# Kernel optimization log

Hardware: AMD Instinct MI355X
Metric: run time of the kernel (lower is better)

Reference implementation:

```python
import jax, jax.numpy as jnp
import numpy as np

E, H, K = 768, 512, 8  # word_emb_size, nhidden, nhead
B, NA, NC = 32, 64, 64


def setup_inputs() -> dict:
    key = jax.random.key(0)
    ks = jax.random.split(key, 8)
    w = lambda k, shape: (jax.random.normal(k, shape, jnp.float32) * 0.02)
    return {
        'he_anchor': jax.random.normal(ks[0], (B, NA, E), jnp.float32),
        'he_pos': jax.random.normal(ks[1], (B, NC, E), jnp.float32),
        'he_neg': jax.random.uniform(ks[2], (B,), jnp.float32),  # SBERT target scores
        'Wa': w(ks[3], (H, E)), 'ba': jnp.zeros((H,), jnp.float32),
        'Wc': w(ks[4], (H, E)), 'bc': jnp.zeros((H,), jnp.float32),
        'Watt': w(ks[5], (K, H)), 'batt': jnp.zeros((K,), jnp.float32),
        'Wscore': w(ks[6], (1, K * H)), 'bscore': jnp.zeros((1,), jnp.float32),
    }


def _score(ha, hc, Wa, ba, Wc, bc, Watt, batt, Wscore, bscore):
    b, na, _ = ha.shape
    A = ha @ Wa.T + ba  # [B,Na,H]  (a2h)
    C = hc @ Wc.T + bc  # [B,Nc,H]  (c2h)
    # self_mul[b,i,j,h] = A[b,i,h]*C[b,j,h]; att logits = h2att(self_mul)
    logits = jnp.einsum('bih,bjh,kh->bkij', A, C, Watt) + batt[None, :, None, None]
    att = jax.nn.softmax(logits.reshape(b, K, -1), axis=-1).reshape(logits.shape)  # [B,K,Na,Nc]
    # per-head bilinear: out[b,k,h] = sum_ij A[b,i,h] * att[b,k,i,j] * C[b,j,h]
    out = jnp.einsum('bih,bkij,bjh->bkh', A, att, C)  # [B,K,H], head-major like torch cat
    score = out.reshape(b, K * H) @ Wscore.T + bscore  # [B,1]
    return score, att


def reference(he_anchor, he_pos, he_neg, Wa, ba, Wc, bc, Watt, batt, Wscore, bscore):
    score_p, att_map = _score(he_anchor, he_pos, Wa, ba, Wc, bc, Watt, batt, Wscore, bscore)
    score_bert = he_neg.reshape(-1, 1)
    loss = jnp.mean((score_p - score_bert) ** 2)  # nn.MSELoss
    return score_p, loss, att_map
```

## Files before the change

### kernel.cpp

```cpp
#include <hip/hip_runtime.h>

#define E_DIM 768

typedef __attribute__((ext_vector_type(8))) short bf16x8;
typedef __attribute__((ext_vector_type(4))) float f32x4;

__device__ __forceinline__ unsigned short f2bf(float f) {
    union { float f; unsigned int u; } v; v.f = f;
    unsigned int u = v.u;
    return (unsigned short)((u + 0x7FFFu + ((u >> 16) & 1u)) >> 16);
}
__device__ __forceinline__ float bfu_lo(unsigned int u) {
    union { unsigned int u; float f; } v; v.u = u << 16; return v.f;
}
__device__ __forceinline__ float bfu_hi(unsigned int u) {
    union { unsigned int u; float f; } v; v.u = u & 0xFFFF0000u; return v.f;
}
__device__ __forceinline__ float bfs(unsigned short s) {
    union { unsigned int u; float f; } v; v.u = ((unsigned int)s) << 16; return v.f;
}
__device__ __forceinline__ unsigned int cvt_pk_bf16(float lo, float hi) {
    unsigned int u;
    asm("v_cvt_pk_bf16_f32 %0, %1, %2" : "=v"(u) : "v"(lo), "v"(hi));
    return u;
}

__global__ __launch_bounds__(512) void k_proj_mfma(
    const float* __restrict__ he_a, const float* __restrict__ Wa, const float* __restrict__ ba,
    const float* __restrict__ he_p, const float* __restrict__ Wc, const float* __restrict__ bc,
    unsigned short* __restrict__ dsts, float* __restrict__ score_acc,
    unsigned int* __restrict__ counter)
{
    __shared__ unsigned short Xs[128 * 40];
    __shared__ unsigned short Wl[64 * 40];
    int t = threadIdx.x;
    int bid = blockIdx.x;
    if (bid == 0) {
        if (t < 32) score_acc[t] = 0.f;
        else if (t == 32) *counter = 0u;
    }
    int which = bid >> 7;
    int loc = bid & 127;
    int mbase = (loc & 15) * 128;
    int hbase = (loc >> 4) * 64;
    const float* Xg = which ? he_p : he_a;
    const float* Wg = which ? Wc : Wa;
    const float* bias = which ? bc : ba;
    int lane = t & 63, w = t >> 6;
    int wr = w >> 1, wc = w & 1;

    int xr0 = t >> 3,          xc0 = t & 7;
    int xr1 = (t + 512) >> 3,  xc1 = t & 7;
    int wrr = t >> 3,          wcc = t & 7;

    float4 p0 = *(const float4*)(Xg + (size_t)(mbase + xr0) * E_DIM + xc0 * 4);
    float4 p1 = *(const float4*)(Xg + (size_t)(mbase + xr1) * E_DIM + xc1 * 4);
    float4 p2 = *(const float4*)(Wg + (size_t)(hbase + wrr) * E_DIM + wcc * 4);

    f32x4 acc[2][2] = {};
    for (int kt = 0; kt < 24; ++kt) {
        __syncthreads();
        *(uint2*)&Xs[xr0 * 40 + xc0 * 4] =
            make_uint2(cvt_pk_bf16(p0.x, p0.y), cvt_pk_bf16(p0.z, p0.w));
        *(uint2*)&Xs[xr1 * 40 + xc1 * 4] =
            make_uint2(cvt_pk_bf16(p1.x, p1.y), cvt_pk_bf16(p1.z, p1.w));
        *(uint2*)&Wl[wrr * 40 + wcc * 4] =
            make_uint2(cvt_pk_bf16(p2.x, p2.y), cvt_pk_bf16(p2.z, p2.w));
        if (kt < 23) {
            int e0 = (kt + 1) * 32;
            p0 = *(const float4*)(Xg + (size_t)(mbase + xr0) * E_DIM + e0 + xc0 * 4);
            p1 = *(const float4*)(Xg + (size_t)(mbase + xr1) * E_DIM + e0 + xc1 * 4);
            p2 = *(const float4*)(Wg + (size_t)(hbase + wrr) * E_DIM + e0 + wcc * 4);
        }
        __syncthreads();
        int ar = lane & 15;
        int k0 = (lane >> 4) * 8;
        bf16x8 af[2], bfr[2];
#pragma unroll
        for (int mi = 0; mi < 2; ++mi)
            af[mi] = *(const bf16x8*)&Xs[(wr * 32 + mi * 16 + ar) * 40 + k0];
#pragma unroll
        for (int ni = 0; ni < 2; ++ni)
            bfr[ni] = *(const bf16x8*)&Wl[(wc * 32 + ni * 16 + ar) * 40 + k0];
#pragma unroll
        for (int mi = 0; mi < 2; ++mi)
#pragma unroll
            for (int ni = 0; ni < 2; ++ni)
                acc[mi][ni] = __builtin_amdgcn_mfma_f32_16x16x32_bf16(
                    af[mi], bfr[ni], acc[mi][ni], 0, 0, 0);
    }
#pragma unroll
    for (int ni = 0; ni < 2; ++ni) {
        int h = hbase + wc * 32 + ni * 16 + (lane & 15);
        float bv = bias[h];
#pragma unroll
        for (int mi = 0; mi < 2; ++mi) {
#pragma unroll
            for (int r = 0; r < 4; ++r) {
                int grow = mbase + wr * 32 + mi * 16 + (lane >> 4) * 4 + r;
                int b = grow >> 6, i = grow & 63;
                float v = acc[mi][ni][r] + bv;
                dsts[(size_t)b * 65536 + (which ? 32768 : 0) + i * 512 + h] = f2bf(v);
            }
        }
    }
}

__global__ __launch_bounds__(512) void k_att_fused(
    float* __restrict__ out, const unsigned short* __restrict__ src,
    const float* __restrict__ Watt, const float* __restrict__ Wsc,
    const float* __restrict__ he_neg, const float* __restrict__ bsc,
    float* __restrict__ score_acc, unsigned int* __restrict__ counter)
{
    __shared__ float red[8];
    __shared__ float sqv[32];
    __shared__ int lastflag;
    int t = threadIdx.x;
    int lane = t & 63, w = t >> 6;
    int rf = w & 3, jh = w >> 2;
    int b = blockIdx.x & 31, k = blockIdx.x >> 5;
    int l15 = lane & 15, lhi = lane >> 4;

    const unsigned short* Ab = src + (size_t)b * 65536;
    const unsigned short* Cb = Ab + 32768;
    const unsigned short* ap  = Ab + (size_t)(rf * 16 + l15) * 512 + lhi * 8;
    const unsigned short* cp0 = Cb + (size_t)(jh * 32 + l15) * 512 + lhi * 8;
    const unsigned short* cp1 = cp0 + 16 * 512;
    const float* wkbase = Watt + k * 512 + lhi * 8;
    const float* wgbase = Wsc  + k * 512 + lhi * 8;

    f32x4 accS[2] = {}, accG[2] = {};
#pragma unroll 2
    for (int ks = 0; ks < 16; ++ks) {
        int h = ks * 32;
        bf16x8 af  = *(const bf16x8*)(ap + h);
        bf16x8 cb0 = *(const bf16x8*)(cp0 + h);
        bf16x8 cb1 = *(const bf16x8*)(cp1 + h);
        float wkv[8], wgv[8];
        *(float4*)&wkv[0] = *(const float4*)(wkbase + h);
        *(float4*)&wkv[4] = *(const float4*)(wkbase + h + 4);
        *(float4*)&wgv[0] = *(const float4*)(wgbase + h);
        *(float4*)&wgv[4] = *(const float4*)(wgbase + h + 4);
        float a[8];
#pragma unroll
        for (int e = 0; e < 8; ++e) a[e] = bfs((unsigned short)af[e]);
        union { unsigned int u[4]; bf16x8 v; } ak, ag;
#pragma unroll
        for (int e2 = 0; e2 < 4; ++e2) {
            ak.u[e2] = cvt_pk_bf16(a[2 * e2] * wkv[2 * e2], a[2 * e2 + 1] * wkv[2 * e2 + 1]);
            ag.u[e2] = cvt_pk_bf16(a[2 * e2] * wgv[2 * e2], a[2 * e2 + 1] * wgv[2 * e2 + 1]);
        }
        accS[0] = __builtin_amdgcn_mfma_f32_16x16x32_bf16(ak.v, cb0, accS[0], 0, 0, 0);
        accS[1] = __builtin_amdgcn_mfma_f32_16x16x32_bf16(ak.v, cb1, accS[1], 0, 0, 0);
        accG[0] = __builtin_amdgcn_mfma_f32_16x16x32_bf16(ag.v, cb0, accG[0], 0, 0, 0);
        accG[1] = __builtin_amdgcn_mfma_f32_16x16x32_bf16(ag.v, cb1, accG[1], 0, 0, 0);
    }

    float lmax = accS[0][0];
#pragma unroll
    for (int ni = 0; ni < 2; ++ni)
#pragma unroll
        for (int r = 0; r < 4; ++r) lmax = fmaxf(lmax, accS[ni][r]);
    float v = lmax;
#pragma unroll
    for (int off = 32; off > 0; off >>= 1) v = fmaxf(v, __shfl_xor(v, off));
    if (lane == 0) red[w] = v;
    __syncthreads();
    float M = red[0];
#pragma unroll
    for (int q = 1; q < 8; ++q) M = fmaxf(M, red[q]);
    __syncthreads();
    float ev[8];
    float lsum = 0.f;
#pragma unroll
    for (int ni = 0; ni < 2; ++ni)
#pragma unroll
        for (int r = 0; r < 4; ++r) {
            float e = __expf(accS[ni][r] - M);
            ev[ni * 4 + r] = e;
            lsum += e;
        }
    v = lsum;
#pragma unroll
    for (int off = 32; off > 0; off >>= 1) v += __shfl_xor(v, off);
    if (lane == 0) red[w] = v;
    __syncthreads();
    float Z = 0.f;
#pragma unroll
    for (int q = 0; q < 8; ++q) Z += red[q];
    float inv = 1.0f / Z;
    __syncthreads();

    float pacc = 0.f;
    float* attk = out + 33 + (size_t)b * 32768 + (size_t)k * 4096;
#pragma unroll
    for (int ni = 0; ni < 2; ++ni) {
        int j = jh * 32 + ni * 16 + l15;
#pragma unroll
        for (int r = 0; r < 4; ++r) {
            int i = rf * 16 + lhi * 4 + r;
            float av = ev[ni * 4 + r] * inv;
            attk[i * 64 + j] = av;
            pacc += av * accG[ni][r];
        }
    }
    v = pacc;
#pragma unroll
    for (int off = 32; off > 0; off >>= 1) v += __shfl_xor(v, off);
    if (lane == 0) red[w] = v;
    __syncthreads();
    if (t == 0) {
        float tot = 0.f;
#pragma unroll
        for (int q = 0; q < 8; ++q) tot += red[q];
        atomicAdd(&score_acc[b], tot);
        __threadfence();
        unsigned int done = atomicAdd(counter, 1u);
        lastflag = (done == 255u) ? 1 : 0;
    }
    __syncthreads();
    if (lastflag) {
        __threadfence();
        if (t < 32) {
            float s = atomicAdd(&score_acc[t], 0.0f) + bsc[0];
            out[t] = s;
            float d = s - he_neg[t];
            sqv[t] = d * d;
        }
        __syncthreads();
        if (t == 0) {
            float l = 0.f;
            for (int q = 0; q < 32; ++q) l += sqv[q];
            out[32] = l * (1.0f / 32.0f);
        }
    }
}

__global__ __launch_bounds__(256) void k_att_valu8(
    float* __restrict__ out, const unsigned int* __restrict__ src,
    const float* __restrict__ Watt, const float* __restrict__ Wsc)
{
    __shared__ unsigned int Al[64 * 260];
    __shared__ unsigned int Cl[64 * 260];
    __shared__ float Wattl[512], Wscl[512];
    __shared__ float red[4];
    int t = threadIdx.x;
    int lane = t & 63, wave = t >> 6;
    int b = blockIdx.x;
    const unsigned int* srcb = src + (size_t)b * 32768;

    for (int s = t; s < 16384; s += 256) {
        int row = s >> 8, hp = s & 255;
        Al[row * 260 + hp] = srcb[s];
        Cl[row * 260 + hp] = srcb[16384 + s];
    }

    int i = t >> 2;
    int jb = (t & 3) * 16;
    float* attreg = out + 33 + (size_t)b * 32768;
    float blocktotal = 0.f;

    for (int k = 0; k < 8; ++k) {
        for (int s = t; s < 512; s += 256) {
            Wattl[s] = Watt[k * 512 + s];
            Wscl[s]  = Wsc[k * 512 + s];
        }
        __syncthreads();
        float sacc[16] = {}, gacc[16] = {};
        const unsigned int* Arow = &Al[i * 260];
        const unsigned int* Crow = &Cl[jb * 260];
        for (int hp = 0; hp < 256; hp += 2) {
            uint2 au = *(const uint2*)&Arow[hp];
            float a0 = bfu_lo(au.x), a1 = bfu_hi(au.x);
            float a2 = bfu_lo(au.y), a3 = bfu_hi(au.y);
            int h0 = hp * 2;
            float4 wk = *(const float4*)&Wattl[h0];
            float4 wg = *(const float4*)&Wscl[h0];
            float ak0 = a0 * wk.x, ak1 = a1 * wk.y, ak2 = a2 * wk.z, ak3 = a3 * wk.w;
            float ag0 = a0 * wg.x, ag1 = a1 * wg.y, ag2 = a2 * wg.z, ag3 = a3 * wg.w;
#pragma unroll
            for (int q = 0; q < 16; ++q) {
                uint2 cu = *(const uint2*)&Crow[q * 260 + hp];
                float c0 = bfu_lo(cu.x), c1 = bfu_hi(cu.x);
                float c2 = bfu_lo(cu.y), c3 = bfu_hi(cu.y);
                sacc[q] = fmaf(ak0, c0, sacc[q]); gacc[q] = fmaf(ag0, c0, gacc[q]);
                sacc[q] = fmaf(ak1, c1, sacc[q]); gacc[q] = fmaf(ag1, c1, gacc[q]);
                sacc[q] = fmaf(ak2, c2, sacc[q]); gacc[q] = fmaf(ag2, c2, gacc[q]);
                sacc[q] = fmaf(ak3, c3, sacc[q]); gacc[q] = fmaf(ag3, c3, gacc[q]);
            }
        }
        float lmax = sacc[0];
#pragma unroll
        for (int e = 1; e < 16; ++e) lmax = fmaxf(lmax, sacc[e]);
        float v = lmax;
#pragma unroll
        for (int off = 32; off > 0; off >>= 1) v = fmaxf(v, __shfl_xor(v, off));
        if (lane == 0) red[wave] = v;
        __syncthreads();
        float M = fmaxf(fmaxf(red[0], red[1]), fmaxf(red[2], red[3]));
        __syncthreads();
        float lsum = 0.f;
#pragma unroll
        for (int e = 0; e < 16; ++e) {
            sacc[e] = __expf(sacc[e] - M);
            lsum += sacc[e];
        }
        v = lsum;
#pragma unroll
        for (int off = 32; off > 0; off >>= 1) v += __shfl_xor(v, off);
        if (lane == 0) red[wave] = v;
        __syncthreads();
        float Z = red[0] + red[1] + red[2] + red[3];
        float inv = 1.0f / Z;
        __syncthreads();
        float pacc = 0.f;
        float* attk = attreg + k * 4096 + i * 64 + jb;
#pragma unroll
        for (int e = 0; e < 16; ++e) {
            float att = sacc[e] * inv;
            attk[e] = att;
            pacc += att * gacc[e];
        }
        v = pacc;
#pragma unroll
        for (int off = 32; off > 0; off >>= 1) v += __shfl_xor(v, off);
        if (lane == 0) red[wave] = v;
        __syncthreads();
        if (t == 0) blocktotal += red[0] + red[1] + red[2] + red[3];
        __syncthreads();
    }
    if (t == 0) out[b] = blocktotal;
}

__global__ __launch_bounds__(64) void k_loss(
    float* __restrict__ out, const float* __restrict__ he_neg,
    const float* __restrict__ bsc)
{
    __shared__ float sq[32];
    int t = threadIdx.x;
    if (t < 32) {
        float s = out[t] + bsc[0];
        out[t] = s;
        float d = s - he_neg[t];
        sq[t] = d * d;
    }
    __syncthreads();
    if (t == 0) {
        float l = 0.f;
        for (int i2 = 0; i2 < 32; ++i2) l += sq[i2];
        out[32] = l * (1.0f / 32.0f);
    }
}

extern "C" void kernel_launch(void* const* d_in, const int* in_sizes, int n_in,
                              void* d_out, int out_size, void* d_ws, size_t ws_size,
                              hipStream_t stream) {
    int iA = 0, iP = 1, iN = 2, iWa = 3, iBa = 4, iWc = 5, iBc = 6, iWatt = 7, iWsc = 9, iBsc = 10;
    if (!(in_sizes[0] == 1572864 && in_sizes[2] == 32)) {
        if (n_in == 11 && in_sizes[0] == 393216 && in_sizes[8] == 1572864) {
            iWa = 0; iWatt = 1; iWc = 2; iWsc = 3; iBa = 4; iBc = 6; iBsc = 7;
            iA = 8; iN = 9; iP = 10;
        }
    }
    const float* he_a  = (const float*)d_in[iA];
    const float* he_p  = (const float*)d_in[iP];
    const float* he_n  = (const float*)d_in[iN];
    const float* Wa    = (const float*)d_in[iWa];
    const float* ba    = (const float*)d_in[iBa];
    const float* Wc    = (const float*)d_in[iWc];
    const float* bc    = (const float*)d_in[iBc];
    const float* Watt  = (const float*)d_in[iWatt];
    const float* Wsc   = (const float*)d_in[iWsc];
    const float* bsc   = (const float*)d_in[iBsc];
    float* out = (float*)d_out;

    size_t need = ((size_t)4 << 20) + 256;
    if (d_ws != nullptr && ws_size >= need) {
        unsigned short* wss = (unsigned short*)d_ws;
        float* score_acc = (float*)((char*)d_ws + ((size_t)4 << 20));
        unsigned int* counter = (unsigned int*)(score_acc + 32);
        k_proj_mfma<<<dim3(256), dim3(512), 0, stream>>>(
            he_a, Wa, ba, he_p, Wc, bc, wss, score_acc, counter);
        k_att_fused<<<dim3(256), dim3(512), 0, stream>>>(
            out, wss, Watt, Wsc, he_n, bsc, score_acc, counter);
    } else {
        unsigned short* region = (unsigned short*)(out + 33);
        static float s_dummy[33];
        (void)s_dummy;
        k_proj_mfma<<<dim3(256), dim3(512), 0, stream>>>(
            he_a, Wa, ba, he_p, Wc, bc, region, (float*)(out), (unsigned int*)(out + 32));
        k_att_valu8<<<dim3(32), dim3(256), 0, stream>>>(out, (unsigned int*)region, Watt, Wsc);
        k_loss<<<dim3(1), dim3(64), 0, stream>>>(out, he_n, bsc);
    }
}
```

Measured before the change: 51.05 us.

## Halve proj block size with larger per-wave tiles, prefetch att loads, remap blocks

The projection kernel now runs 256 threads per block, and each wave computes a 64x32 output tile (4x2 MFMA fragments) instead of 32x32. This raises register reuse of the B fragments and cuts per-block thread count. The attention kernel fully unrolls its K loop with register double-buffering of the A/C/weight loads, and remaps block indices so neighbouring blocks share batches differently for cache locality. The cost is more registers per thread, and the unrolled prefetch may raise register pressure.

```diff
diff --git a/kernel.cpp b/kernel.cpp
--- a/kernel.cpp
+++ b/kernel.cpp
@@ -25,7 +25,7 @@
     return u;
 }
 
-__global__ __launch_bounds__(512) void k_proj_mfma(
+__global__ __launch_bounds__(256) void k_proj_mfma(
     const float* __restrict__ he_a, const float* __restrict__ Wa, const float* __restrict__ ba,
     const float* __restrict__ he_p, const float* __restrict__ Wc, const float* __restrict__ bc,
     unsigned short* __restrict__ dsts, float* __restrict__ score_acc,
@@ -33,8 +33,8 @@
 {
     __shared__ unsigned short Xs[128 * 40];
     __shared__ unsigned short Wl[64 * 40];
+    int bid = blockIdx.x;
     int t = threadIdx.x;
-    int bid = blockIdx.x;
     if (bid == 0) {
         if (t < 32) score_acc[t] = 0.f;
         else if (t == 32) *counter = 0u;
@@ -49,41 +49,61 @@
     int lane = t & 63, w = t >> 6;
     int wr = w >> 1, wc = w & 1;
 
-    int xr0 = t >> 3,          xc0 = t & 7;
-    int xr1 = (t + 512) >> 3,  xc1 = t & 7;
-    int wrr = t >> 3,          wcc = t & 7;
-
-    float4 p0 = *(const float4*)(Xg + (size_t)(mbase + xr0) * E_DIM + xc0 * 4);
-    float4 p1 = *(const float4*)(Xg + (size_t)(mbase + xr1) * E_DIM + xc1 * 4);
-    float4 p2 = *(const float4*)(Wg + (size_t)(hbase + wrr) * E_DIM + wcc * 4);
-
-    f32x4 acc[2][2] = {};
+    float4 xr4[4];
+    float4 wr4[2];
+#pragma unroll
+    for (int it = 0; it < 4; ++it) {
+        int idx = t + it * 256; int row = idx >> 3, c4 = idx & 7;
+        xr4[it] = *(const float4*)(Xg + (size_t)(mbase + row) * E_DIM + c4 * 4);
+    }
+#pragma unroll
+    for (int it = 0; it < 2; ++it) {
+        int idx = t + it * 256; int row = idx >> 3, c4 = idx & 7;
+        wr4[it] = *(const float4*)(Wg + (size_t)(hbase + row) * E_DIM + c4 * 4);
+    }
+
+    f32x4 acc[4][2] = {};
     for (int kt = 0; kt < 24; ++kt) {
         __syncthreads();
-        *(uint2*)&Xs[xr0 * 40 + xc0 * 4] =
-            make_uint2(cvt_pk_bf16(p0.x, p0.y), cvt_pk_bf16(p0.z, p0.w));
-        *(uint2*)&Xs[xr1 * 40 + xc1 * 4] =
-            make_uint2(cvt_pk_bf16(p1.x, p1.y), cvt_pk_bf16(p1.z, p1.w));
-        *(uint2*)&Wl[wrr * 40 + wcc * 4] =
-            make_uint2(cvt_pk_bf16(p2.x, p2.y), cvt_pk_bf16(p2.z, p2.w));
+#pragma unroll
+        for (int it = 0; it < 4; ++it) {
+            int idx = t + it * 256; int row = idx >> 3, c4 = idx & 7;
+            uint2 u = make_uint2(cvt_pk_bf16(xr4[it].x, xr4[it].y),
+                                 cvt_pk_bf16(xr4[it].z, xr4[it].w));
+            *(uint2*)&Xs[row * 40 + c4 * 4] = u;
+        }
+#pragma unroll
+        for (int it = 0; it < 2; ++it) {
+            int idx = t + it * 256; int row = idx >> 3, c4 = idx & 7;
+            uint2 u = make_uint2(cvt_pk_bf16(wr4[it].x, wr4[it].y),
+                                 cvt_pk_bf16(wr4[it].z, wr4[it].w));
+            *(uint2*)&Wl[row * 40 + c4 * 4] = u;
+        }
         if (kt < 23) {
             int e0 = (kt + 1) * 32;
-            p0 = *(const float4*)(Xg + (size_t)(mbase + xr0) * E_DIM + e0 + xc0 * 4);
-            p1 = *(const float4*)(Xg + (size_t)(mbase + xr1) * E_DIM + e0 + xc1 * 4);
-            p2 = *(const float4*)(Wg + (size_t)(hbase + wrr) * E_DIM + e0 + wcc * 4);
+#pragma unroll
+            for (int it = 0; it < 4; ++it) {
+                int idx = t + it * 256; int row = idx >> 3, c4 = idx & 7;
+                xr4[it] = *(const float4*)(Xg + (size_t)(mbase + row) * E_DIM + e0 + c4 * 4);
+            }
+#pragma unroll
+            for (int it = 0; it < 2; ++it) {
+                int idx = t + it * 256; int row = idx >> 3, c4 = idx & 7;
+                wr4[it] = *(const float4*)(Wg + (size_t)(hbase + row) * E_DIM + e0 + c4 * 4);
+            }
         }
         __syncthreads();
         int ar = lane & 15;
         int k0 = (lane >> 4) * 8;
-        bf16x8 af[2], bfr[2];
-#pragma unroll
-        for (int mi = 0; mi < 2; ++mi)
-            af[mi] = *(const bf16x8*)&Xs[(wr * 32 + mi * 16 + ar) * 40 + k0];
+        bf16x8 af[4], bfr[2];
+#pragma unroll
+        for (int mi = 0; mi < 4; ++mi)
+            af[mi] = *(const bf16x8*)&Xs[(wr * 64 + mi * 16 + ar) * 40 + k0];
 #pragma unroll
         for (int ni = 0; ni < 2; ++ni)
             bfr[ni] = *(const bf16x8*)&Wl[(wc * 32 + ni * 16 + ar) * 40 + k0];
 #pragma unroll
-        for (int mi = 0; mi < 2; ++mi)
+        for (int mi = 0; mi < 4; ++mi)
 #pragma unroll
             for (int ni = 0; ni < 2; ++ni)
                 acc[mi][ni] = __builtin_amdgcn_mfma_f32_16x16x32_bf16(
@@ -94,10 +114,10 @@
         int h = hbase + wc * 32 + ni * 16 + (lane & 15);
         float bv = bias[h];
 #pragma unroll
-        for (int mi = 0; mi < 2; ++mi) {
+        for (int mi = 0; mi < 4; ++mi) {
 #pragma unroll
             for (int r = 0; r < 4; ++r) {
-                int grow = mbase + wr * 32 + mi * 16 + (lane >> 4) * 4 + r;
+                int grow = mbase + wr * 64 + mi * 16 + (lane >> 4) * 4 + r;
                 int b = grow >> 6, i = grow & 63;
                 float v = acc[mi][ni][r] + bv;
                 dsts[(size_t)b * 65536 + (which ? 32768 : 0) + i * 512 + h] = f2bf(v);
@@ -118,7 +138,10 @@
     int t = threadIdx.x;
     int lane = t & 63, w = t >> 6;
     int rf = w & 3, jh = w >> 2;
-    int b = blockIdx.x & 31, k = blockIdx.x >> 5;
+    int bid = blockIdx.x;
+    int x = bid & 7, s = bid >> 3;
+    int b = 2 * x + (s & 1) + 16 * ((s >> 1) & 1);
+    int k = s >> 2;
     int l15 = lane & 15, lhi = lane >> 4;
 
     const unsigned short* Ab = src + (size_t)b * 65536;
@@ -126,34 +149,49 @@
     const unsigned short* ap  = Ab + (size_t)(rf * 16 + l15) * 512 + lhi * 8;
     const unsigned short* cp0 = Cb + (size_t)(jh * 32 + l15) * 512 + lhi * 8;
     const unsigned short* cp1 = cp0 + 16 * 512;
-    const float* wkbase = Watt + k * 512 + lhi * 8;
-    const float* wgbase = Wsc  + k * 512 + lhi * 8;
+    const float* wkb = Watt + k * 512 + lhi * 8;
+    const float* wgb = Wsc  + k * 512 + lhi * 8;
+
+    bf16x8 af_[2], c0_[2], c1_[2];
+    float4 wk0_[2], wk1_[2], wg0_[2], wg1_[2];
+    af_[0]  = *(const bf16x8*)(ap);
+    c0_[0]  = *(const bf16x8*)(cp0);
+    c1_[0]  = *(const bf16x8*)(cp1);
+    wk0_[0] = *(const float4*)(wkb);
+    wk1_[0] = *(const float4*)(wkb + 4);
+    wg0_[0] = *(const float4*)(wgb);
+    wg1_[0] = *(const float4*)(wgb + 4);
 
     f32x4 accS[2] = {}, accG[2] = {};
-#pragma unroll 2
+#pragma unroll
     for (int ks = 0; ks < 16; ++ks) {
-        int h = ks * 32;
-        bf16x8 af  = *(const bf16x8*)(ap + h);
-        bf16x8 cb0 = *(const bf16x8*)(cp0 + h);
-        bf16x8 cb1 = *(const bf16x8*)(cp1 + h);
+        int cur = ks & 1, nxt = cur ^ 1;
+        if (ks < 15) {
+            int h = (ks + 1) * 32;
+            af_[nxt]  = *(const bf16x8*)(ap + h);
+            c0_[nxt]  = *(const bf16x8*)(cp0 + h);
+            c1_[nxt]  = *(const bf16x8*)(cp1 + h);
+            wk0_[nxt] = *(const float4*)(wkb + h);
+            wk1_[nxt] = *(const float4*)(wkb + h + 4);
+            wg0_[nxt] = *(const float4*)(wgb + h);
+            wg1_[nxt] = *(const float4*)(wgb + h + 4);
+        }
+        float a[8];
+#pragma unroll
+        for (int e = 0; e < 8; ++e) a[e] = bfs((unsigned short)af_[cur][e]);
         float wkv[8], wgv[8];
-        *(float4*)&wkv[0] = *(const float4*)(wkbase + h);
-        *(float4*)&wkv[4] = *(const float4*)(wkbase + h + 4);
-        *(float4*)&wgv[0] = *(const float4*)(wgbase + h);
-        *(float4*)&wgv[4] = *(const float4*)(wgbase + h + 4);
-        float a[8];
-#pragma unroll
-        for (int e = 0; e < 8; ++e) a[e] = bfs((unsigned short)af[e]);
+        *(float4*)&wkv[0] = wk0_[cur]; *(float4*)&wkv[4] = wk1_[cur];
+        *(float4*)&wgv[0] = wg0_[cur]; *(float4*)&wgv[4] = wg1_[cur];
         union { unsigned int u[4]; bf16x8 v; } ak, ag;
 #pragma unroll
         for (int e2 = 0; e2 < 4; ++e2) {
             ak.u[e2] = cvt_pk_bf16(a[2 * e2] * wkv[2 * e2], a[2 * e2 + 1] * wkv[2 * e2 + 1]);
             ag.u[e2] = cvt_pk_bf16(a[2 * e2] * wgv[2 * e2], a[2 * e2 + 1] * wgv[2 * e2 + 1]);
         }
-        accS[0] = __builtin_amdgcn_mfma_f32_16x16x32_bf16(ak.v, cb0, accS[0], 0, 0, 0);
-        accS[1] = __builtin_amdgcn_mfma_f32_16x16x32_bf16(ak.v, cb1, accS[1], 0, 0, 0);
-        accG[0] = __builtin_amdgcn_mfma_f32_16x16x32_bf16(ag.v, cb0, accG[0], 0, 0, 0);
-        accG[1] = __builtin_amdgcn_mfma_f32_16x16x32_bf16(ag.v, cb1, accG[1], 0, 0, 0);
+        accS[0] = __builtin_amdgcn_mfma_f32_16x16x32_bf16(ak.v, c0_[cur], accS[0], 0, 0, 0);
+        accS[1] = __builtin_amdgcn_mfma_f32_16x16x32_bf16(ak.v, c1_[cur], accS[1], 0, 0, 0);
+        accG[0] = __builtin_amdgcn_mfma_f32_16x16x32_bf16(ag.v, c0_[cur], accG[0], 0, 0, 0);
+        accG[1] = __builtin_amdgcn_mfma_f32_16x16x32_bf16(ag.v, c1_[cur], accG[1], 0, 0, 0);
     }
 
     float lmax = accS[0][0];
@@ -222,9 +260,9 @@
     if (lastflag) {
         __threadfence();
         if (t < 32) {
-            float s = atomicAdd(&score_acc[t], 0.0f) + bsc[0];
-            out[t] = s;
-            float d = s - he_neg[t];
+            float sc = atomicAdd(&score_acc[t], 0.0f) + bsc[0];
+            out[t] = sc;
+            float d = sc - he_neg[t];
             sqv[t] = d * d;
         }
         __syncthreads();
@@ -379,15 +417,13 @@
         unsigned short* wss = (unsigned short*)d_ws;
         float* score_acc = (float*)((char*)d_ws + ((size_t)4 << 20));
         unsigned int* counter = (unsigned int*)(score_acc + 32);
-        k_proj_mfma<<<dim3(256), dim3(512), 0, stream>>>(
+        k_proj_mfma<<<dim3(256), dim3(256), 0, stream>>>(
             he_a, Wa, ba, he_p, Wc, bc, wss, score_acc, counter);
         k_att_fused<<<dim3(256), dim3(512), 0, stream>>>(
             out, wss, Watt, Wsc, he_n, bsc, score_acc, counter);
     } else {
         unsigned short* region = (unsigned short*)(out + 33);
-        static float s_dummy[33];
-        (void)s_dummy;
-        k_proj_mfma<<<dim3(256), dim3(512), 0, stream>>>(
+        k_proj_mfma<<<dim3(256), dim3(256), 0, stream>>>(
             he_a, Wa, ba, he_p, Wc, bc, region, (float*)(out), (unsigned int*)(out + 32));
         k_att_valu8<<<dim3(32), dim3(256), 0, stream>>>(out, (unsigned int*)region, Watt, Wsc);
         k_loss<<<dim3(1), dim3(64), 0, stream>>>(out, he_n, bsc);
```

Result: faster. 49.00 us (-4.0%).
